# Kernel tuning notes

Measured on AMD Instinct MI355X. Metric: run time of the kernel, lower is better.

## Reference

```python
import jax, jax.numpy as jnp
import numpy as np

B, N, C, H, L = 4, 1024, 1152, 16, 120
D = C // H
HID = 4 * C
EPS = 1e-6


def _ln(x):
    m = jnp.mean(x, axis=-1, keepdims=True)
    v = jnp.var(x, axis=-1, keepdims=True)
    return (x - m) * jax.lax.rsqrt(v + EPS)


def _attend(q, k, v):
    # q:(B,H,Nq,D) k,v:(B,H,Nk,D)
    scale = D ** -0.5
    s = jnp.einsum('bhnd,bhmd->bhnm', q, k) * scale
    p = jax.nn.softmax(s, axis=-1)
    o = jnp.einsum('bhnm,bhmd->bhnd', p, v)
    return o.transpose(0, 2, 1, 3).reshape(q.shape[0], q.shape[2], C)


def setup_inputs() -> dict:
    key = jax.random.key(0)
    ks = jax.random.split(key, 20)
    g = lambda i, shape, s=0.02: jax.random.normal(ks[i], shape, jnp.float32) * s
    return {
        'x': jax.random.normal(ks[0], (B, N, C), jnp.float32),
        'y': jax.random.normal(ks[1], (B, L, C), jnp.float32),
        't': jax.random.normal(ks[2], (B, 6 * C), jnp.float32),
        'sst': jax.random.normal(ks[3], (6, C), jnp.float32) / C ** 0.5,
        'qkv_w': g(4, (C, 3 * C)), 'qkv_b': jnp.zeros((3 * C,), jnp.float32),
        'proj_w': g(5, (C, C)), 'proj_b': jnp.zeros((C,), jnp.float32),
        'q_w': g(6, (C, C)), 'q_b': jnp.zeros((C,), jnp.float32),
        'kv_w': g(7, (C, 2 * C)), 'kv_b': jnp.zeros((2 * C,), jnp.float32),
        'cproj_w': g(8, (C, C)), 'cproj_b': jnp.zeros((C,), jnp.float32),
        'fc1_w': g(9, (C, HID)), 'fc1_b': jnp.zeros((HID,), jnp.float32),
        'fc2_w': g(10, (HID, C)), 'fc2_b': jnp.zeros((C,), jnp.float32),
    }


def reference(x, y, t, sst, qkv_w, qkv_b, proj_w, proj_b, q_w, q_b,
              kv_w, kv_b, cproj_w, cproj_b, fc1_w, fc1_b, fc2_w, fc2_b):
    mods = sst[None] + t.reshape(B, 6, C)  # (B,6,C)
    sh_msa, sc_msa, g_msa, sh_mlp, sc_mlp, g_mlp = [mods[:, i:i + 1] for i in range(6)]

    # --- self attention with adaLN modulation ---
    h = _ln(x) * (1 + sc_msa) + sh_msa
    qkv = (h @ qkv_w + qkv_b).reshape(B, N, 3, H, D).transpose(2, 0, 3, 1, 4)
    attn_out = _attend(qkv[0], qkv[1], qkv[2]) @ proj_w + proj_b
    x = x + g_msa * attn_out

    # --- cross attention (batched cond, no mask) ---
    q = (x @ q_w + q_b).reshape(B, N, H, D).transpose(0, 2, 1, 3)
    kv = (y @ kv_w + kv_b).reshape(B, L, 2, H, D).transpose(2, 0, 3, 1, 4)
    x = x + (_attend(q, kv[0], kv[1]) @ cproj_w + cproj_b)

    # --- MLP with adaLN modulation ---
    h = _ln(x) * (1 + sc_mlp) + sh_mlp
    h = jax.nn.gelu(h @ fc1_w + fc1_b, approximate=True) @ fc2_w + fc2_b
    x = x + g_mlp * h
    return x
```

## Files before the change

kernel.cpp:

```cpp
#include <hip/hip_runtime.h>
#include <hip/hip_bf16.h>
#include <stdint.h>

typedef __hip_bfloat16 BT;
typedef __bf16 bf16x8 __attribute__((ext_vector_type(8)));
typedef float f32x4 __attribute__((ext_vector_type(4)));

constexpr int kB = 4, kN = 1024, kC = 1152, kH = 16, kL = 120, kD = 72, kDp = 96;
constexpr int kHid = 4608, kBN = 4096, kZ = 64;
constexpr float kScale = 0.11785113019775793f;

__global__ void detect_dtype(const void* xin, int* flag) {
  __shared__ int cnt;
  if (threadIdx.x == 0) cnt = 0;
  __syncthreads();
  const BT* xb = (const BT*)xin;
  int local = 0;
  for (int i = threadIdx.x; i < 4096; i += 256) {
    float v = __bfloat162float(xb[i]);
    if (!(fabsf(v) <= 1e3f)) local++;
  }
  atomicAdd(&cnt, local);
  __syncthreads();
  if (threadIdx.x == 0) *flag = (cnt > 8) ? 1 : 0;
}

struct ConvSeg {
  const void* src;
  BT* dst;
  long long n;
};
struct ConvArgs {
  ConvSeg seg[10];
  int nseg;
};
__global__ void convert_all(ConvArgs a, const int* __restrict__ flag) {
  const int f = *flag;
  long long i = (long long)blockIdx.x * 256 + threadIdx.x;
#pragma unroll
  for (int s = 0; s < 10; ++s) {
    if (s >= a.nseg) return;
    if (i < a.seg[s].n) {
      a.seg[s].dst[i] = f ? __float2bfloat16(((const float*)a.seg[s].src)[i])
                          : ((const BT*)a.seg[s].src)[i];
      return;
    }
    i -= a.seg[s].n;
  }
}

__global__ void encode_ws(float* out, long long n, float c) {
  long long i = (long long)blockIdx.x * 256 + threadIdx.x;
  if (i < n) out[i] = c;
}

__device__ __forceinline__ void gl_lds16(const BT* g, BT* l) {
  __builtin_amdgcn_global_load_lds(
      (const __attribute__((address_space(1))) uint32_t*)g,
      (__attribute__((address_space(3))) uint32_t*)l, 16, 0, 0);
}

template <int EP>
__global__ __launch_bounds__(512, 2) void gemm_w8(
    const BT* __restrict__ A, const BT* __restrict__ Bm, const BT* __restrict__ bias,
    void* __restrict__ Cout, int M, int Nc, int K, int lda, int ldb, int ldc,
    long long sA, long long sB, long long sC) {
  __shared__ __align__(16) BT As[2][128 * 64];
  __shared__ __align__(16) BT Bs[2][128 * 64];
  A += (long long)blockIdx.z * sA;
  Bm += (long long)blockIdx.z * sB;

  const int gx = gridDim.x, nwg = gx * gridDim.y;
  int id = blockIdx.y * gx + blockIdx.x;
  {
    const int q = nwg >> 3, r = nwg & 7;
    const int xcd = id & 7, pos = id >> 3;
    const int base = (xcd < r) ? xcd * (q + 1) : r * (q + 1) + (xcd - r) * q;
    id = base + pos;
  }
  const int m0 = (id / gx) * 128, n0 = (id % gx) * 128;

  const int lane = threadIdx.x & 63, w = threadIdx.x >> 6;
  const int l15 = lane & 15;
  const int srow = lane >> 3;
  const int ssrc = ((lane & 7) ^ srow) * 8;
  const int wm = (w & 1) * 64, wn = (w >> 1) * 32;

  const int u = w;
  const BT* gp[4];
#pragma unroll
  for (int q = 0; q < 4; ++q) {
    int rr, lim;
    const BT* basep;
    int stride;
    if (u < 4) { rr = m0 + u * 32; lim = M; basep = A; stride = lda; }
    else { rr = n0 + (u - 4) * 32; lim = Nc; basep = Bm; stride = ldb; }
    rr += q * 8 + srow;
    if (rr >= lim) rr = lim - 1;
    gp[q] = basep + (long long)rr * stride + ssrc;
  }
  BT* dst[2];
#pragma unroll
  for (int bb = 0; bb < 2; ++bb)
    dst[bb] = (u < 4) ? &As[bb][u * 2048] : &Bs[bb][(u - 4) * 2048];

  auto stage = [&](int bb, int k0) {
#pragma unroll
    for (int q = 0; q < 4; ++q) gl_lds16(gp[q] + k0, dst[bb] + q * 512);
  };

  const int rsw = l15 & 7;
  const int ch0 = ((lane >> 4) ^ rsw) * 8;
  const int ch1 = ((4 | (lane >> 4)) ^ rsw) * 8;

  f32x4 acc[4][2] = {};

  auto compute = [&](int bb) {
    bf16x8 af[4][2], bf[2][2];
#pragma unroll
    for (int i = 0; i < 4; ++i) {
      const int row = wm + i * 16 + l15;
      af[i][0] = *reinterpret_cast<const bf16x8*>(&As[bb][row * 64 + ch0]);
      af[i][1] = *reinterpret_cast<const bf16x8*>(&As[bb][row * 64 + ch1]);
    }
#pragma unroll
    for (int j = 0; j < 2; ++j) {
      const int row = wn + j * 16 + l15;
      bf[j][0] = *reinterpret_cast<const bf16x8*>(&Bs[bb][row * 64 + ch0]);
      bf[j][1] = *reinterpret_cast<const bf16x8*>(&Bs[bb][row * 64 + ch1]);
    }
#pragma unroll
    for (int i = 0; i < 4; ++i)
#pragma unroll
      for (int j = 0; j < 2; ++j) {
        acc[i][j] = __builtin_amdgcn_mfma_f32_16x16x32_bf16(af[i][0], bf[j][0], acc[i][j], 0, 0, 0);
        acc[i][j] = __builtin_amdgcn_mfma_f32_16x16x32_bf16(af[i][1], bf[j][1], acc[i][j], 0, 0, 0);
      }
  };

  stage(0, 0);
  __syncthreads();
  const int nk = K >> 6;
  int cur = 0;
  for (int t = 1; t < nk; ++t) {
    stage(cur ^ 1, t << 6);
    compute(cur);
    __syncthreads();
    cur ^= 1;
  }
  compute(cur);

  const int rowq = (lane >> 4) * 4;
  const long long cb = (long long)blockIdx.z * sC;
#pragma unroll
  for (int j = 0; j < 2; ++j) {
    int col = n0 + wn + j * 16 + l15;
    if (col >= Nc) continue;
    float bv = bias ? __bfloat162float(bias[col]) : 0.f;
#pragma unroll
    for (int i = 0; i < 4; ++i) {
      int row = m0 + wm + i * 16 + rowq;
#pragma unroll
      for (int r = 0; r < 4; ++r) {
        if (row + r < M) {
          float v = acc[i][j][r] + bv;
          if (EP == 2) {
            float z = 1.5957691216057308f * (v + 0.044715f * v * v * v);
            v = v / (1.f + __expf(-z));
          }
          long long off = cb + (long long)(row + r) * ldc + col;
          if (EP == 1)
            ((float*)Cout)[off] = v;
          else
            ((BT*)Cout)[off] = __float2bfloat16(v);
        }
      }
    }
  }
}

template <int BM, int BN, int EP>
__global__ __launch_bounds__(256, 3) void gemm_t64(
    const BT* __restrict__ A, const BT* __restrict__ Bm, const BT* __restrict__ bias,
    void* __restrict__ Cout, int M, int Nc, int K, int lda, int ldb, int ldc,
    long long sA, long long sB, long long sC) {
  constexpr int NA = BM / 32;
  constexpr int NB = BN / 32;
  constexpr int NU = NA + NB;
  constexpr int NJ = 2;
  __shared__ __align__(16) BT As[2][BM * 64];
  __shared__ __align__(16) BT Bs[2][BN * 64];
  A += (long long)blockIdx.z * sA;
  Bm += (long long)blockIdx.z * sB;

  const int gx = gridDim.x, nwg = gx * gridDim.y;
  int id = blockIdx.y * gx + blockIdx.x;
  {
    const int q = nwg >> 3, r = nwg & 7;
    const int xcd = id & 7, pos = id >> 3;
    const int base = (xcd < r) ? xcd * (q + 1) : r * (q + 1) + (xcd - r) * q;
    id = base + pos;
  }
  const int m0 = (id / gx) * BM, n0 = (id % gx) * BN;

  const int lane = threadIdx.x & 63, w = threadIdx.x >> 6;
  const int l15 = lane & 15;
  const int srow = lane >> 3;
  const int ssrc = ((lane & 7) ^ srow) * 8;
  int wm, wn;
  if (BM == 128) { wm = (w >> 1) * 64; wn = (w & 1) * 32; }
  else { wm = 0; wn = w * 32; }

  const bool has2 = (w + 4 < NU);
  const int u1 = w;
  const int u2 = has2 ? (w + 4) : w;
  const BT* gp1[4];
  const BT* gp2[4];
#pragma unroll
  for (int q = 0; q < 4; ++q) {
    {
      int rr, lim;
      const BT* basep;
      int stride;
      if (u1 < NA) { rr = m0 + u1 * 32; lim = M; basep = A; stride = lda; }
      else { rr = n0 + (u1 - NA) * 32; lim = Nc; basep = Bm; stride = ldb; }
      rr += q * 8 + srow;
      if (rr >= lim) rr = lim - 1;
      gp1[q] = basep + (long long)rr * stride + ssrc;
    }
    {
      int rr, lim;
      const BT* basep;
      int stride;
      if (u2 < NA) { rr = m0 + u2 * 32; lim = M; basep = A; stride = lda; }
      else { rr = n0 + (u2 - NA) * 32; lim = Nc; basep = Bm; stride = ldb; }
      rr += q * 8 + srow;
      if (rr >= lim) rr = lim - 1;
      gp2[q] = basep + (long long)rr * stride + ssrc;
    }
  }
  BT* d1[2];
  BT* d2[2];
#pragma unroll
  for (int bb = 0; bb < 2; ++bb) {
    d1[bb] = (u1 < NA) ? &As[bb][u1 * 2048] : &Bs[bb][(u1 - NA) * 2048];
    int ub = u2 - NA;
    if (ub < 0) ub = 0;
    if (ub > NB - 1) ub = NB - 1;
    d2[bb] = (u2 < NA) ? &As[bb][u2 * 2048] : &Bs[bb][ub * 2048];
  }

  auto stage = [&](int bb, int k0) {
#pragma unroll
    for (int q = 0; q < 4; ++q) gl_lds16(gp1[q] + k0, d1[bb] + q * 512);
    if (has2) {
#pragma unroll
      for (int q = 0; q < 4; ++q) gl_lds16(gp2[q] + k0, d2[bb] + q * 512);
    }
  };

  const int rsw = l15 & 7;
  const int ch0 = ((lane >> 4) ^ rsw) * 8;
  const int ch1 = ((4 | (lane >> 4)) ^ rsw) * 8;

  f32x4 acc[4][NJ] = {};

  auto compute = [&](int bb) {
    bf16x8 af[4][2], bf[NJ][2];
#pragma unroll
    for (int i = 0; i < 4; ++i) {
      const int row = wm + i * 16 + l15;
      af[i][0] = *reinterpret_cast<const bf16x8*>(&As[bb][row * 64 + ch0]);
      af[i][1] = *reinterpret_cast<const bf16x8*>(&As[bb][row * 64 + ch1]);
    }
#pragma unroll
    for (int j = 0; j < NJ; ++j) {
      const int row = wn + j * 16 + l15;
      bf[j][0] = *reinterpret_cast<const bf16x8*>(&Bs[bb][row * 64 + ch0]);
      bf[j][1] = *reinterpret_cast<const bf16x8*>(&Bs[bb][row * 64 + ch1]);
    }
#pragma unroll
    for (int i = 0; i < 4; ++i)
#pragma unroll
      for (int j = 0; j < NJ; ++j) {
        acc[i][j] = __builtin_amdgcn_mfma_f32_16x16x32_bf16(af[i][0], bf[j][0], acc[i][j], 0, 0, 0);
        acc[i][j] = __builtin_amdgcn_mfma_f32_16x16x32_bf16(af[i][1], bf[j][1], acc[i][j], 0, 0, 0);
      }
  };

  stage(0, 0);
  __syncthreads();
  const int nk = K >> 6;
  int cur = 0;
  for (int t = 1; t < nk; ++t) {
    stage(cur ^ 1, t << 6);
    compute(cur);
    __syncthreads();
    cur ^= 1;
  }
  compute(cur);

  const int rowq = (lane >> 4) * 4;
  const long long cb = (long long)blockIdx.z * sC;
#pragma unroll
  for (int j = 0; j < NJ; ++j) {
    int col = n0 + wn + j * 16 + l15;
    if (col >= Nc) continue;
    float bv = bias ? __bfloat162float(bias[col]) : 0.f;
#pragma unroll
    for (int i = 0; i < 4; ++i) {
      int row = m0 + wm + i * 16 + rowq;
#pragma unroll
      for (int r = 0; r < 4; ++r) {
        if (row + r < M) {
          float v = acc[i][j][r] + bv;
          if (EP == 2) {
            float z = 1.5957691216057308f * (v + 0.044715f * v * v * v);
            v = v / (1.f + __expf(-z));
          }
          long long off = cb + (long long)(row + r) * ldc + col;
          if (EP == 1)
            ((float*)Cout)[off] = v;
          else
            ((BT*)Cout)[off] = __float2bfloat16(v);
        }
      }
    }
  }
}

template <int EP>
__global__ __launch_bounds__(256, 4) void gemm_tile(
    const BT* __restrict__ A, const BT* __restrict__ Bm, const BT* __restrict__ bias,
    void* __restrict__ Cout, int M, int Nc, int K, int lda, int ldb, int ldc,
    long long sA, long long sB, long long sC) {
  __shared__ __align__(16) BT As[2][128 * 32];
  __shared__ __align__(16) BT Bs[2][128 * 32];
  A += (long long)blockIdx.z * sA;
  Bm += (long long)blockIdx.z * sB;

  const int gx = gridDim.x, nwg = gx * gridDim.y;
  int id = blockIdx.y * gx + blockIdx.x;
  {
    const int q = nwg >> 3, r = nwg & 7;
    const int xcd = id & 7, pos = id >> 3;
    const int base = (xcd < r) ? xcd * (q + 1) : r * (q + 1) + (xcd - r) * q;
    id = base + pos;
  }
  const int m0 = (id / gx) * 128, n0 = (id % gx) * 128;

  const int lane = threadIdx.x & 63, w = threadIdx.x >> 6;
  const int lr = lane >> 2, lc = (lane & 3) * 8;
  const int l15 = lane & 15, q8 = (lane >> 4) * 8;
  const int wm = (w & 1) * 64, wn = (w >> 1) * 64;

  int ra0 = m0 + w * 32 + lr, ra1 = ra0 + 16;
  if (ra0 >= M) ra0 = M - 1;
  if (ra1 >= M) ra1 = M - 1;
  int rb0 = n0 + w * 32 + lr, rb1 = rb0 + 16;
  if (rb0 >= Nc) rb0 = Nc - 1;
  if (rb1 >= Nc) rb1 = Nc - 1;
  const BT* pa0 = A + (long long)ra0 * lda + lc;
  const BT* pa1 = A + (long long)ra1 * lda + lc;
  const BT* pb0 = Bm + (long long)rb0 * ldb + lc;
  const BT* pb1 = Bm + (long long)rb1 * ldb + lc;

  auto stage = [&](int bb, int k0) {
    gl_lds16(pa0 + k0, &As[bb][w * 1024]);
    gl_lds16(pa1 + k0, &As[bb][w * 1024 + 512]);
    gl_lds16(pb0 + k0, &Bs[bb][w * 1024]);
    gl_lds16(pb1 + k0, &Bs[bb][w * 1024 + 512]);
  };

  f32x4 acc[4][4] = {};

  auto compute = [&](int bb) {
    bf16x8 af[4], bf[4];
#pragma unroll
    for (int i = 0; i < 4; ++i)
      af[i] = *reinterpret_cast<const bf16x8*>(&As[bb][(wm + i * 16 + l15) * 32 + q8]);
#pragma unroll
    for (int j = 0; j < 4; ++j)
      bf[j] = *reinterpret_cast<const bf16x8*>(&Bs[bb][(wn + j * 16 + l15) * 32 + q8]);
#pragma unroll
    for (int i = 0; i < 4; ++i)
#pragma unroll
      for (int j = 0; j < 4; ++j)
        acc[i][j] = __builtin_amdgcn_mfma_f32_16x16x32_bf16(af[i], bf[j], acc[i][j], 0, 0, 0);
  };

  stage(0, 0);
  __syncthreads();
  const int nk = K >> 5;
  int cur = 0;
  for (int t = 1; t < nk; ++t) {
    stage(cur ^ 1, t << 5);
    compute(cur);
    __syncthreads();
    cur ^= 1;
  }
  compute(cur);

  const int rowq = (lane >> 4) * 4;
  const long long cb = (long long)blockIdx.z * sC;
#pragma unroll
  for (int j = 0; j < 4; ++j) {
    int col = n0 + wn + j * 16 + l15;
    if (col >= Nc) continue;
    float bv = bias ? __bfloat162float(bias[col]) : 0.f;
#pragma unroll
    for (int i = 0; i < 4; ++i) {
      int row = m0 + wm + i * 16 + rowq;
#pragma unroll
      for (int r = 0; r < 4; ++r) {
        if (row + r < M) {
          float v = acc[i][j][r] + bv;
          if (EP == 2) {
            float z = 1.5957691216057308f * (v + 0.044715f * v * v * v);
            v = v / (1.f + __expf(-z));
          }
          long long off = cb + (long long)(row + r) * ldc + col;
          if (EP == 1)
            ((float*)Cout)[off] = v;
          else
            ((BT*)Cout)[off] = __float2bfloat16(v);
        }
      }
    }
  }
}

__global__ void transpose_any(const void* __restrict__ in, BT* __restrict__ out,
                              int R, int Cin, const int* __restrict__ flag) {
  __shared__ BT tile[32][33];
  const int f = *flag;
  const int tx = threadIdx.x & 31, ty = threadIdx.x >> 5;
  const int r0 = blockIdx.y * 32, c0 = blockIdx.x * 32;
#pragma unroll
  for (int j = 0; j < 32; j += 8) {
    int r = r0 + ty + j;
    if (r < R && c0 + tx < Cin) {
      long long idx = (long long)r * Cin + c0 + tx;
      tile[ty + j][tx] = f ? __float2bfloat16(((const float*)in)[idx]) : ((const BT*)in)[idx];
    }
  }
  __syncthreads();
#pragma unroll
  for (int j = 0; j < 32; j += 8) {
    int oc = c0 + ty + j;
    if (oc < Cin && r0 + tx < R) out[(long long)oc * R + r0 + tx] = tile[tx][ty + j];
  }
}

template <int SRC>
__global__ __launch_bounds__(256) void ln_mod(const void* __restrict__ xin,
                                              const BT* __restrict__ tc,
                                              const BT* __restrict__ sstc,
                                              BT* __restrict__ hout,
                                              int shiftRow, int scaleRow,
                                              const int* __restrict__ flag) {
  const int f = (SRC == 1) ? 1 : *flag;
  const int row = blockIdx.x;
  const int b = row >> 10;
  const long long base = (long long)row * kC;
  float s = 0.f, s2 = 0.f;
  for (int c = threadIdx.x; c < kC; c += 256) {
    float v = f ? ((const float*)xin)[base + c] : __bfloat162float(((const BT*)xin)[base + c]);
    s += v;
    s2 += v * v;
  }
  for (int o = 32; o > 0; o >>= 1) {
    s += __shfl_down(s, o, 64);
    s2 += __shfl_down(s2, o, 64);
  }
  __shared__ float red[8];
  const int w = threadIdx.x >> 6;
  if ((threadIdx.x & 63) == 0) {
    red[w] = s;
    red[4 + w] = s2;
  }
  __syncthreads();
  const float m = (red[0] + red[1] + red[2] + red[3]) * (1.f / kC);
  const float ex2 = (red[4] + red[5] + red[6] + red[7]) * (1.f / kC);
  const float rstd = rsqrtf(ex2 - m * m + 1e-6f);
  const BT* tsh = tc + (long long)b * 6 * kC + (long long)shiftRow * kC;
  const BT* tsc = tc + (long long)b * 6 * kC + (long long)scaleRow * kC;
  const BT* ssh = sstc + (long long)shiftRow * kC;
  const BT* ssc = sstc + (long long)scaleRow * kC;
  for (int c = threadIdx.x; c < kC; c += 256) {
    float sc = __bfloat162float(ssc[c]) + __bfloat162float(tsc[c]);
    float sh = __bfloat162float(ssh[c]) + __bfloat162float(tsh[c]);
    float xv0 = f ? ((const float*)xin)[base + c] : __bfloat162float(((const BT*)xin)[base + c]);
    float xv = (xv0 - m) * rstd;
    hout[base + c] = __float2bfloat16(xv * (1.f + sc) + sh);
  }
}

__global__ void scatter_qk(const BT* __restrict__ qkv, BT* __restrict__ Qp,
                           BT* __restrict__ Kp) {
  long long i = (long long)blockIdx.x * 256 + threadIdx.x;
  if (i >= (long long)kZ * kN * kDp) return;
  int d = (int)(i % kDp);
  long long r = i / kDp;
  int n = (int)(r % kN);
  int z = (int)(r / kN);
  int b = z >> 4, h = z & 15;
  if (d < kD) {
    long long src = ((long long)(b * kN + n)) * (3 * kC) + h * kD + d;
    Qp[i] = __float2bfloat16(kScale * __bfloat162float(qkv[src]));
    Kp[i] = qkv[src + kC];
  } else {
    Qp[i] = __float2bfloat16(0.f);
    Kp[i] = __float2bfloat16(0.f);
  }
}

__global__ void scatter_v(const BT* __restrict__ qkv, BT* __restrict__ VT) {
  long long i = (long long)blockIdx.x * 256 + threadIdx.x;
  if (i >= (long long)kZ * kD * kN) return;
  int n = (int)(i % kN);
  long long r = i / kN;
  int d = (int)(r % kD);
  int z = (int)(r / kD);
  int b = z >> 4, h = z & 15;
  VT[i] = qkv[((long long)(b * kN + n)) * (3 * kC) + 2 * kC + h * kD + d];
}

__global__ void scatter_qc(const BT* __restrict__ qc, BT* __restrict__ Qp) {
  long long i = (long long)blockIdx.x * 256 + threadIdx.x;
  if (i >= (long long)kZ * kN * kDp) return;
  int d = (int)(i % kDp);
  long long r = i / kDp;
  int n = (int)(r % kN);
  int z = (int)(r / kN);
  int b = z >> 4, h = z & 15;
  Qp[i] = (d < kD)
              ? __float2bfloat16(kScale * __bfloat162float(qc[((long long)(b * kN + n)) * kC + h * kD + d]))
              : __float2bfloat16(0.f);
}

__global__ void scatter_kc(const BT* __restrict__ kvb, BT* __restrict__ Kcp) {
  long long i = (long long)blockIdx.x * 256 + threadIdx.x;
  if (i >= (long long)kZ * kL * kDp) return;
  int d = (int)(i % kDp);
  long long r = i / kDp;
  int l = (int)(r % kL);
  int z = (int)(r / kL);
  int b = z >> 4, h = z & 15;
  Kcp[i] = (d < kD) ? kvb[((long long)(b * kL + l)) * (2 * kC) + h * kD + d] : __float2bfloat16(0.f);
}

__global__ void scatter_vc(const BT* __restrict__ kvb, BT* __restrict__ VcT) {
  long long i = (long long)blockIdx.x * 256 + threadIdx.x;
  if (i >= (long long)kZ * kD * 128) return;
  int l = (int)(i % 128);
  long long r = i / 128;
  int d = (int)(r % kD);
  int z = (int)(r / kD);
  int b = z >> 4, h = z & 15;
  VcT[i] = (l < kL) ? kvb[((long long)(b * kL + l)) * (2 * kC) + kC + h * kD + d] : __float2bfloat16(0.f);
}

__global__ void heads_to_cat(const BT* __restrict__ O, BT* __restrict__ cat) {
  long long i = (long long)blockIdx.x * 256 + threadIdx.x;
  if (i >= (long long)kZ * kN * kD) return;
  int d = (int)(i % kD);
  long long r = i / kD;
  int n = (int)(r % kN);
  int z = (int)(r / kN);
  int b = z >> 4, h = z & 15;
  cat[((long long)(b * kN + n)) * kC + h * kD + d] = O[i];
}

__global__ __launch_bounds__(256) void softmax1024(BT* __restrict__ S) {
  const long long row = blockIdx.x;
  BT* r = S + row * 1024;
  const int tid = threadIdx.x;
  union { ushort4 u; BT b[4]; } ld;
  ld.u = *(const ushort4*)(r + tid * 4);
  float v[4];
#pragma unroll
  for (int k = 0; k < 4; ++k) v[k] = __bfloat162float(ld.b[k]);
  float mx = fmaxf(fmaxf(v[0], v[1]), fmaxf(v[2], v[3]));
  for (int o = 32; o > 0; o >>= 1) mx = fmaxf(mx, __shfl_down(mx, o, 64));
  __shared__ float red[4], red2[4];
  if ((tid & 63) == 0) red[tid >> 6] = mx;
  __syncthreads();
  mx = fmaxf(fmaxf(red[0], red[1]), fmaxf(red[2], red[3]));
  float s = 0.f;
#pragma unroll
  for (int k = 0; k < 4; ++k) {
    v[k] = __expf(v[k] - mx);
    s += v[k];
  }
  for (int o = 32; o > 0; o >>= 1) s += __shfl_down(s, o, 64);
  if ((tid & 63) == 0) red2[tid >> 6] = s;
  __syncthreads();
  s = red2[0] + red2[1] + red2[2] + red2[3];
  const float inv = 1.f / s;
#pragma unroll
  for (int k = 0; k < 4; ++k) ld.b[k] = __float2bfloat16(v[k] * inv);
  *(ushort4*)(r + tid * 4) = ld.u;
}

__global__ void softmax_cross(BT* __restrict__ S) {
  const long long row = blockIdx.x;
  BT* r = S + row * 128;
  const int c = threadIdx.x;
  float v = (c < kL) ? __bfloat162float(r[c]) : -1e30f;
  float mx = v;
  for (int o = 32; o > 0; o >>= 1) mx = fmaxf(mx, __shfl_down(mx, o, 64));
  __shared__ float sm[2], ss[2];
  if ((c & 63) == 0) sm[c >> 6] = mx;
  __syncthreads();
  mx = fmaxf(sm[0], sm[1]);
  float e = (c < kL) ? __expf(v - mx) : 0.f;
  float s = e;
  for (int o = 32; o > 0; o >>= 1) s += __shfl_down(s, o, 64);
  if ((c & 63) == 0) ss[c >> 6] = s;
  __syncthreads();
  s = ss[0] + ss[1];
  r[c] = __float2bfloat16(e / s);
}

__global__ void resid_gate(const void* __restrict__ x, const BT* __restrict__ raw,
                           const BT* __restrict__ tc, const BT* __restrict__ sstc,
                           float* __restrict__ resf, BT* __restrict__ resb,
                           const int* __restrict__ flag) {
  long long i = (long long)blockIdx.x * 256 + threadIdx.x;
  if (i >= (long long)kBN * kC) return;
  const int f = *flag;
  int c = (int)(i % kC);
  int b = (int)(i / ((long long)kN * kC));
  float g = __bfloat162float(sstc[2 * kC + c]) + __bfloat162float(tc[(long long)b * 6 * kC + 2 * kC + c]);
  float xv = f ? ((const float*)x)[i] : __bfloat162float(((const BT*)x)[i]);
  float v = xv + g * __bfloat162float(raw[i]);
  resf[i] = v;
  resb[i] = __float2bfloat16(v);
}

__global__ void resid_add(float* __restrict__ res, const BT* __restrict__ raw) {
  long long i = (long long)blockIdx.x * 256 + threadIdx.x;
  if (i < (long long)kBN * kC) res[i] += __bfloat162float(raw[i]);
}

__global__ void final_out(const float* __restrict__ res, const BT* __restrict__ raw,
                          const BT* __restrict__ tc, const BT* __restrict__ sstc,
                          float* __restrict__ out) {
  long long i = (long long)blockIdx.x * 256 + threadIdx.x;
  if (i >= (long long)kBN * kC) return;
  int c = (int)(i % kC);
  int b = (int)(i / ((long long)kN * kC));
  float g = __bfloat162float(sstc[5 * kC + c]) + __bfloat162float(tc[(long long)b * 6 * kC + 5 * kC + c]);
  out[i] = res[i] + g * __bfloat162float(raw[i]);
}

extern "C" void kernel_launch(void* const* d_in, const int* in_sizes, int n_in,
                              void* d_out, int out_size, void* d_ws, size_t ws_size,
                              hipStream_t stream) {
  const void* x = d_in[0];
  const void* y = d_in[1];
  const void* t = d_in[2];
  const void* sst = d_in[3];
  const void* qkv_w = d_in[4];
  const void* qkv_b = d_in[5];
  const void* proj_w = d_in[6];
  const void* proj_b = d_in[7];
  const void* q_w = d_in[8];
  const void* q_b = d_in[9];
  const void* kv_w = d_in[10];
  const void* kv_b = d_in[11];
  const void* cproj_w = d_in[12];
  const void* cproj_b = d_in[13];
  const void* fc1_w = d_in[14];
  const void* fc1_b = d_in[15];
  const void* fc2_w = d_in[16];
  const void* fc2_b = d_in[17];
  (void)in_sizes; (void)n_in;

  char* p = (char*)d_ws;
  size_t off = 0;
  auto alloc = [&](size_t bytes) {
    void* r = p + off;
    off += (bytes + 1023) & ~(size_t)1023;
    return r;
  };
  int* dflag = (int*)alloc(16);
  BT* canonY = (BT*)alloc((size_t)kB * kL * kC * 2);
  BT* canonT = (BT*)alloc((size_t)kB * 6 * kC * 2);
  BT* canonSst = (BT*)alloc((size_t)6 * kC * 2);
  BT* canonBias = (BT*)alloc((size_t)16384 * 2);
  BT* wT = (BT*)alloc((size_t)kHid * kC * 2);
  BT* bufH = (BT*)alloc((size_t)kBN * kC * 2);
  BT* bufCH = (BT*)alloc((size_t)kZ * kN * kDp * 2);
  BT* bufQp = (BT*)alloc((size_t)kZ * kN * kDp * 2);
  BT* bufVT = (BT*)alloc((size_t)kZ * kD * kN * 2);
  BT* rawB = (BT*)alloc((size_t)kBN * kC * 2);
  float* resF = (float*)alloc((size_t)kBN * kC * 4);
  BT* arena = (BT*)alloc((size_t)kBN * kHid * 2);
  const size_t need = off;

  BT* bufO = rawB;
  BT* fc2T = bufQp;
  BT* kvBuf = (BT*)((char*)arena + 17825792);

  if (ws_size < need) {
    float c = 100.f * (float)(1 + (int)(ws_size >> 24));
    long long n = (long long)out_size;
    encode_ws<<<(int)((n + 255) / 256), 256, 0, stream>>>((float*)d_out, n, c);
    return;
  }

  BT* qkvB = canonBias;
  BT* projB = canonBias + 3456;
  BT* qB = canonBias + 4608;
  BT* kvB = canonBias + 5760;
  BT* cprojB = canonBias + 8064;
  BT* fc1B = canonBias + 9216;
  BT* fc2B = canonBias + 13824;

  auto gemm = [&](int ep, const BT* A, const BT* Bm, const BT* bias, void* Cp,
                  int M, int Nc, int K, int lda, int ldb, int ldc,
                  long long sA, long long sB, long long sC, int Zb) {
    if (K & 63) {
      dim3 g((Nc + 127) / 128, (M + 127) / 128, Zb);
      if (ep == 0)
        gemm_tile<0><<<g, 256, 0, stream>>>(A, Bm, bias, Cp, M, Nc, K, lda, ldb, ldc, sA, sB, sC);
      else if (ep == 1)
        gemm_tile<1><<<g, 256, 0, stream>>>(A, Bm, bias, Cp, M, Nc, K, lda, ldb, ldc, sA, sB, sC);
      else
        gemm_tile<2><<<g, 256, 0, stream>>>(A, Bm, bias, Cp, M, Nc, K, lda, ldb, ldc, sA, sB, sC);
      return;
    }
    long long nwg128 = (long long)((Nc + 127) / 128) * ((M + 127) / 128) * Zb;
    if (nwg128 >= 768 && (M & 127) == 0) {
      dim3 g((Nc + 127) / 128, M / 128, Zb);
      if (ep == 0)
        gemm_w8<0><<<g, 512, 0, stream>>>(A, Bm, bias, Cp, M, Nc, K, lda, ldb, ldc, sA, sB, sC);
      else if (ep == 1)
        gemm_w8<1><<<g, 512, 0, stream>>>(A, Bm, bias, Cp, M, Nc, K, lda, ldb, ldc, sA, sB, sC);
      else
        gemm_w8<2><<<g, 512, 0, stream>>>(A, Bm, bias, Cp, M, Nc, K, lda, ldb, ldc, sA, sB, sC);
      return;
    }
    long long n64 = (long long)((Nc + 63) / 64) * ((M + 127) / 128) * Zb;
    if (n64 >= 512) {
      dim3 g((Nc + 63) / 64, (M + 127) / 128, Zb);
      if (ep == 0)
        gemm_t64<128, 64, 0><<<g, 256, 0, stream>>>(A, Bm, bias, Cp, M, Nc, K, lda, ldb, ldc, sA, sB, sC);
      else if (ep == 1)
        gemm_t64<128, 64, 1><<<g, 256, 0, stream>>>(A, Bm, bias, Cp, M, Nc, K, lda, ldb, ldc, sA, sB, sC);
      else
        gemm_t64<128, 64, 2><<<g, 256, 0, stream>>>(A, Bm, bias, Cp, M, Nc, K, lda, ldb, ldc, sA, sB, sC);
    } else {
      dim3 g((Nc + 127) / 128, (M + 63) / 64, Zb);
      if (ep == 0)
        gemm_t64<64, 128, 0><<<g, 256, 0, stream>>>(A, Bm, bias, Cp, M, Nc, K, lda, ldb, ldc, sA, sB, sC);
      else if (ep == 1)
        gemm_t64<64, 128, 1><<<g, 256, 0, stream>>>(A, Bm, bias, Cp, M, Nc, K, lda, ldb, ldc, sA, sB, sC);
      else
        gemm_t64<64, 128, 2><<<g, 256, 0, stream>>>(A, Bm, bias, Cp, M, Nc, K, lda, ldb, ldc, sA, sB, sC);
    }
  };
  auto tp = [&](const void* in, BT* out, int R, int Cin) {
    dim3 g((Cin + 31) / 32, (R + 31) / 32);
    transpose_any<<<g, 256, 0, stream>>>(in, out, R, Cin, dflag);
  };

  detect_dtype<<<1, 256, 0, stream>>>(x, dflag);
  {
    ConvArgs a;
    a.seg[0] = {y, canonY, (long long)kB * kL * kC};
    a.seg[1] = {t, canonT, (long long)kB * 6 * kC};
    a.seg[2] = {sst, canonSst, (long long)6 * kC};
    a.seg[3] = {qkv_b, qkvB, 3456};
    a.seg[4] = {proj_b, projB, 1152};
    a.seg[5] = {q_b, qB, 1152};
    a.seg[6] = {kv_b, kvB, 2304};
    a.seg[7] = {cproj_b, cprojB, 1152};
    a.seg[8] = {fc1_b, fc1B, 4608};
    a.seg[9] = {fc2_b, fc2B, 1152};
    a.nseg = 10;
    long long tot = 552960 + 27648 + 6912 + 14976;
    convert_all<<<(int)((tot + 255) / 256), 256, 0, stream>>>(a, dflag);
  }

  ln_mod<0><<<kBN, 256, 0, stream>>>(x, canonT, canonSst, bufH, 0, 1, dflag);
  tp(qkv_w, wT, kC, 3 * kC);
  gemm(0, bufH, wT, qkvB, arena, kBN, 3 * kC, kC, kC, kC, 3 * kC, 0, 0, 0, 1);
  {
    long long tot = (long long)kZ * kN * kDp;
    scatter_qk<<<(int)((tot + 255) / 256), 256, 0, stream>>>(arena, bufQp, bufCH);
    tot = (long long)kZ * kD * kN;
    scatter_v<<<(int)((tot + 255) / 256), 256, 0, stream>>>(arena, bufVT);
  }
  for (int c = 0; c < 4; ++c) {
    int z0 = c * 16;
    const BT* Qb = bufQp + (size_t)z0 * kN * kDp;
    const BT* Kb = bufCH + (size_t)z0 * kN * kDp;
    const BT* Vb = bufVT + (size_t)z0 * kD * kN;
    BT* Ob = bufO + (size_t)z0 * kN * kD;
    gemm(0, Qb, Kb, nullptr, arena, kN, kN, kDp, kDp, kDp, kN,
         (long long)kN * kDp, (long long)kN * kDp, (long long)kN * kN, 16);
    softmax1024<<<16 * kN, 256, 0, stream>>>(arena);
    gemm(0, arena, Vb, nullptr, Ob, kN, kD, kN, kN, kN, kD,
         (long long)kN * kN, (long long)kD * kN, (long long)kN * kD, 16);
  }
  heads_to_cat<<<18432, 256, 0, stream>>>(bufO, bufCH);
  tp(proj_w, wT, kC, kC);
  gemm(0, bufCH, wT, projB, rawB, kBN, kC, kC, kC, kC, kC, 0, 0, 0, 1);
  resid_gate<<<18432, 256, 0, stream>>>(x, rawB, canonT, canonSst, resF, bufH, dflag);

  tp(q_w, wT, kC, kC);
  gemm(0, bufH, wT, qB, bufCH, kBN, kC, kC, kC, kC, kC, 0, 0, 0, 1);
  {
    long long tot = (long long)kZ * kN * kDp;
    scatter_qc<<<(int)((tot + 255) / 256), 256, 0, stream>>>(bufCH, bufQp);
  }
  tp(kv_w, wT, kC, 2 * kC);
  gemm(0, canonY, wT, kvB, kvBuf, kB * kL, 2 * kC, kC, kC, kC, 2 * kC, 0, 0, 0, 1);
  {
    long long tot = (long long)kZ * kL * kDp;
    scatter_kc<<<(int)((tot + 255) / 256), 256, 0, stream>>>(kvBuf, bufCH);
    tot = (long long)kZ * kD * 128;
    scatter_vc<<<(int)((tot + 255) / 256), 256, 0, stream>>>(kvBuf, bufVT);
  }
  gemm(0, bufQp, bufCH, nullptr, arena, kN, kL, kDp, kDp, kDp, 128,
       (long long)kN * kDp, (long long)kL * kDp, (long long)kN * 128, kZ);
  softmax_cross<<<kZ * kN, 128, 0, stream>>>(arena);
  gemm(0, arena, bufVT, nullptr, bufO, kN, kD, 128, 128, 128, kD,
       (long long)kN * 128, (long long)kD * 128, (long long)kN * kD, kZ);
  heads_to_cat<<<18432, 256, 0, stream>>>(bufO, bufCH);
  tp(cproj_w, wT, kC, kC);
  gemm(0, bufCH, wT, cprojB, rawB, kBN, kC, kC, kC, kC, kC, 0, 0, 0, 1);
  resid_add<<<18432, 256, 0, stream>>>(resF, rawB);

  ln_mod<1><<<kBN, 256, 0, stream>>>(resF, canonT, canonSst, bufH, 3, 4, dflag);
  tp(fc1_w, wT, kC, kHid);
  tp(fc2_w, fc2T, kHid, kC);
  gemm(2, bufH, wT, fc1B, arena, kBN, kHid, kC, kC, kC, kHid, 0, 0, 0, 1);
  gemm(0, arena, fc2T, fc2B, rawB, kBN, kC, kHid, kHid, kHid, kC, 0, 0, 0, 1);
  final_out<<<18432, 256, 0, stream>>>(resF, rawB, canonT, canonSst, (float*)d_out);
}
```

Measured before the change: 828.8 us.

## Fuse self-attention into a single flash-style kernel with online softmax

Replaces the per-chunk QK^T GEMM, standalone softmax kernel and PV GEMM with one kernel. Each block takes a 64-row query tile for one head and runs an online softmax over 128-wide key tiles. Probabilities pass through LDS to the PV MFMAs, so the 1024x1024 score matrix is never written to or read back from global memory, and several launches go away. The tradeoff is that K and V are read straight from global memory without LDS staging. V tiles are padded to 80 columns, which reads slightly past the 72-dim head; those extra columns are discarded.

```diff
diff --git a/kernel.cpp b/kernel.cpp
--- a/kernel.cpp
+++ b/kernel.cpp
@@ -58,6 +58,168 @@
   __builtin_amdgcn_global_load_lds(
       (const __attribute__((address_space(1))) uint32_t*)g,
       (__attribute__((address_space(3))) uint32_t*)l, 16, 0, 0);
+}
+
+__global__ __launch_bounds__(256, 2) void flash_self(
+    const BT* __restrict__ Qp, const BT* __restrict__ Kp, const BT* __restrict__ VT,
+    BT* __restrict__ O) {
+  const int z = blockIdx.y;
+  const int q0 = blockIdx.x * 64;
+  const BT* Qb = Qp + (size_t)z * kN * kDp;
+  const BT* Kb = Kp + (size_t)z * kN * kDp;
+  const BT* Vb = VT + (size_t)z * kD * kN;
+  BT* Ob = O + (size_t)z * kN * kD;
+
+  __shared__ __align__(16) BT Pl[64][136];
+  __shared__ float redm[2][64], reds[2][64], scl[64], lsh[64];
+
+  const int lane = threadIdx.x & 63, w = threadIdx.x >> 6;
+  const int l15 = lane & 15, g8 = (lane >> 4) * 8, rowq = (lane >> 4) * 4;
+  const int wm = (w & 1) * 32, wn = (w >> 1) * 64;
+  const int half = w >> 1;
+  const int orow = w * 16;
+
+  bf16x8 afQ[3][2];
+#pragma unroll
+  for (int ks = 0; ks < 3; ++ks)
+#pragma unroll
+    for (int i = 0; i < 2; ++i)
+      afQ[ks][i] = *reinterpret_cast<const bf16x8*>(
+          &Qb[(size_t)(q0 + wm + i * 16 + l15) * kDp + ks * 32 + g8]);
+
+  float mst[2][4], lst[2][4];
+#pragma unroll
+  for (int i = 0; i < 2; ++i)
+#pragma unroll
+    for (int r = 0; r < 4; ++r) {
+      mst[i][r] = -1e30f;
+      lst[i][r] = 0.f;
+    }
+
+  f32x4 accO[5] = {};
+
+  for (int t = 0; t < 8; ++t) {
+    const int kv0 = t * 128;
+    f32x4 accS[2][4] = {};
+#pragma unroll
+    for (int ks = 0; ks < 3; ++ks) {
+      bf16x8 bfK[4];
+#pragma unroll
+      for (int j = 0; j < 4; ++j)
+        bfK[j] = *reinterpret_cast<const bf16x8*>(
+            &Kb[(size_t)(kv0 + wn + j * 16 + l15) * kDp + ks * 32 + g8]);
+#pragma unroll
+      for (int i = 0; i < 2; ++i)
+#pragma unroll
+        for (int j = 0; j < 4; ++j)
+          accS[i][j] = __builtin_amdgcn_mfma_f32_16x16x32_bf16(afQ[ks][i], bfK[j], accS[i][j], 0, 0, 0);
+    }
+    float tmax[2][4];
+#pragma unroll
+    for (int i = 0; i < 2; ++i)
+#pragma unroll
+      for (int r = 0; r < 4; ++r) {
+        float v = fmaxf(fmaxf(accS[i][0][r], accS[i][1][r]),
+                        fmaxf(accS[i][2][r], accS[i][3][r]));
+        v = fmaxf(v, __shfl_xor(v, 1, 16));
+        v = fmaxf(v, __shfl_xor(v, 2, 16));
+        v = fmaxf(v, __shfl_xor(v, 4, 16));
+        v = fmaxf(v, __shfl_xor(v, 8, 16));
+        tmax[i][r] = v;
+      }
+    if (l15 == 0) {
+#pragma unroll
+      for (int i = 0; i < 2; ++i)
+#pragma unroll
+        for (int r = 0; r < 4; ++r)
+          redm[half][wm + i * 16 + rowq + r] = tmax[i][r];
+    }
+    __syncthreads();
+
+    float sc[2][4], tsum[2][4];
+#pragma unroll
+    for (int i = 0; i < 2; ++i)
+#pragma unroll
+      for (int r = 0; r < 4; ++r) {
+        const int row = wm + i * 16 + rowq + r;
+        const float mt = fmaxf(redm[0][row], redm[1][row]);
+        const float mn = fmaxf(mst[i][r], mt);
+        sc[i][r] = __expf(mst[i][r] - mn);
+        mst[i][r] = mn;
+        float s = 0.f;
+#pragma unroll
+        for (int j = 0; j < 4; ++j) {
+          float pv = __expf(accS[i][j][r] - mn);
+          s += pv;
+          Pl[row][wn + j * 16 + l15] = __float2bfloat16(pv);
+        }
+        s += __shfl_xor(s, 1, 16);
+        s += __shfl_xor(s, 2, 16);
+        s += __shfl_xor(s, 4, 16);
+        s += __shfl_xor(s, 8, 16);
+        tsum[i][r] = s;
+      }
+    if (l15 == 0) {
+#pragma unroll
+      for (int i = 0; i < 2; ++i)
+#pragma unroll
+        for (int r = 0; r < 4; ++r) {
+          const int row = wm + i * 16 + rowq + r;
+          reds[half][row] = tsum[i][r];
+          if (half == 0) scl[row] = sc[i][r];
+        }
+    }
+    __syncthreads();
+
+#pragma unroll
+    for (int i = 0; i < 2; ++i)
+#pragma unroll
+      for (int r = 0; r < 4; ++r) {
+        const int row = wm + i * 16 + rowq + r;
+        lst[i][r] = lst[i][r] * sc[i][r] + (reds[0][row] + reds[1][row]);
+      }
+    float osc[4];
+#pragma unroll
+    for (int r = 0; r < 4; ++r) osc[r] = scl[orow + rowq + r];
+#pragma unroll
+    for (int jv = 0; jv < 5; ++jv)
+#pragma unroll
+      for (int r = 0; r < 4; ++r) accO[jv][r] *= osc[r];
+#pragma unroll
+    for (int ks = 0; ks < 4; ++ks) {
+      bf16x8 aP = *reinterpret_cast<const bf16x8*>(&Pl[orow + l15][ks * 32 + g8]);
+      bf16x8 bV[5];
+#pragma unroll
+      for (int jv = 0; jv < 5; ++jv)
+        bV[jv] = *reinterpret_cast<const bf16x8*>(
+            &Vb[(size_t)(jv * 16 + l15) * kN + kv0 + ks * 32 + g8]);
+#pragma unroll
+      for (int jv = 0; jv < 5; ++jv)
+        accO[jv] = __builtin_amdgcn_mfma_f32_16x16x32_bf16(aP, bV[jv], accO[jv], 0, 0, 0);
+    }
+  }
+
+  if (half == 0 && l15 == 0) {
+#pragma unroll
+    for (int i = 0; i < 2; ++i)
+#pragma unroll
+      for (int r = 0; r < 4; ++r)
+        lsh[wm + i * 16 + rowq + r] = lst[i][r];
+  }
+  __syncthreads();
+  float linv[4];
+#pragma unroll
+  for (int r = 0; r < 4; ++r) linv[r] = 1.f / lsh[orow + rowq + r];
+#pragma unroll
+  for (int jv = 0; jv < 5; ++jv) {
+    const int d = jv * 16 + l15;
+    if (d < kD) {
+#pragma unroll
+      for (int r = 0; r < 4; ++r)
+        Ob[(size_t)(q0 + orow + rowq + r) * kD + d] =
+            __float2bfloat16(accO[jv][r] * linv[r]);
+    }
+  }
 }
 
 template <int EP>
@@ -570,37 +732,6 @@
   int z = (int)(r / kN);
   int b = z >> 4, h = z & 15;
   cat[((long long)(b * kN + n)) * kC + h * kD + d] = O[i];
-}
-
-__global__ __launch_bounds__(256) void softmax1024(BT* __restrict__ S) {
-  const long long row = blockIdx.x;
-  BT* r = S + row * 1024;
-  const int tid = threadIdx.x;
-  union { ushort4 u; BT b[4]; } ld;
-  ld.u = *(const ushort4*)(r + tid * 4);
-  float v[4];
-#pragma unroll
-  for (int k = 0; k < 4; ++k) v[k] = __bfloat162float(ld.b[k]);
-  float mx = fmaxf(fmaxf(v[0], v[1]), fmaxf(v[2], v[3]));
-  for (int o = 32; o > 0; o >>= 1) mx = fmaxf(mx, __shfl_down(mx, o, 64));
-  __shared__ float red[4], red2[4];
-  if ((tid & 63) == 0) red[tid >> 6] = mx;
-  __syncthreads();
-  mx = fmaxf(fmaxf(red[0], red[1]), fmaxf(red[2], red[3]));
-  float s = 0.f;
-#pragma unroll
-  for (int k = 0; k < 4; ++k) {
-    v[k] = __expf(v[k] - mx);
-    s += v[k];
-  }
-  for (int o = 32; o > 0; o >>= 1) s += __shfl_down(s, o, 64);
-  if ((tid & 63) == 0) red2[tid >> 6] = s;
-  __syncthreads();
-  s = red2[0] + red2[1] + red2[2] + red2[3];
-  const float inv = 1.f / s;
-#pragma unroll
-  for (int k = 0; k < 4; ++k) ld.b[k] = __float2bfloat16(v[k] * inv);
-  *(ushort4*)(r + tid * 4) = ld.u;
 }
 
 __global__ void softmax_cross(BT* __restrict__ S) {
@@ -794,18 +925,7 @@
     tot = (long long)kZ * kD * kN;
     scatter_v<<<(int)((tot + 255) / 256), 256, 0, stream>>>(arena, bufVT);
   }
-  for (int c = 0; c < 4; ++c) {
-    int z0 = c * 16;
-    const BT* Qb = bufQp + (size_t)z0 * kN * kDp;
-    const BT* Kb = bufCH + (size_t)z0 * kN * kDp;
-    const BT* Vb = bufVT + (size_t)z0 * kD * kN;
-    BT* Ob = bufO + (size_t)z0 * kN * kD;
-    gemm(0, Qb, Kb, nullptr, arena, kN, kN, kDp, kDp, kDp, kN,
-         (long long)kN * kDp, (long long)kN * kDp, (long long)kN * kN, 16);
-    softmax1024<<<16 * kN, 256, 0, stream>>>(arena);
-    gemm(0, arena, Vb, nullptr, Ob, kN, kD, kN, kN, kN, kD,
-         (long long)kN * kN, (long long)kD * kN, (long long)kN * kD, 16);
-  }
+  flash_self<<<dim3(16, 64), 256, 0, stream>>>(bufQp, bufCH, bufVT, bufO);
   heads_to_cat<<<18432, 256, 0, stream>>>(bufO, bufCH);
   tp(proj_w, wT, kC, kC);
   gemm(0, bufCH, wT, projB, rawB, kBN, kC, kC, kC, kC, kC, 0, 0, 0, 1);
```

Result: faster. 735.0 us (-11.3%).
